# Performance work log

Measured on AMD Instinct MI355X. Metric: run time of the kernel, lower is better.

The kernel has to match this reference:

```python
import jax, jax.numpy as jnp
import numpy as np

HIDDEN = 2048
NUM_HEADS = 16
HEAD_DIM = HIDDEN // NUM_HEADS
INTER = 8192
EPS = 1e-6


def setup_inputs() -> dict:
    key = jax.random.key(0)
    ks = jax.random.split(key, 10)
    s = 0.02
    return {
        "x": jax.random.normal(ks[0], (2, 2048, HIDDEN), dtype=jnp.float32),
        "w_ln1": jnp.ones((HIDDEN,), dtype=jnp.float32),
        "wq": jax.random.normal(ks[1], (HIDDEN, HIDDEN), dtype=jnp.float32) * s,
        "wk": jax.random.normal(ks[2], (HIDDEN, HIDDEN), dtype=jnp.float32) * s,
        "wv": jax.random.normal(ks[3], (HIDDEN, HIDDEN), dtype=jnp.float32) * s,
        "wo": jax.random.normal(ks[4], (HIDDEN, HIDDEN), dtype=jnp.float32) * s,
        "w_ln2": jnp.ones((HIDDEN,), dtype=jnp.float32),
        "wg": jax.random.normal(ks[5], (INTER, HIDDEN), dtype=jnp.float32) * s,
        "wu": jax.random.normal(ks[6], (INTER, HIDDEN), dtype=jnp.float32) * s,
        "wd": jax.random.normal(ks[7], (HIDDEN, INTER), dtype=jnp.float32) * s,
    }


def rmsnorm(x, w):
    rms = jnp.sqrt(jnp.mean(x * x, axis=-1, keepdims=True) + EPS)
    return x / rms * w


def attention(x, wq, wk, wv, wo):
    B, T, C = x.shape
    # weights are [out, in] (torch Linear convention) -> x @ W.T
    q = (x @ wq.T).reshape(B, T, NUM_HEADS, HEAD_DIM)
    k = (x @ wk.T).reshape(B, T, NUM_HEADS, HEAD_DIM)
    v = (x @ wv.T).reshape(B, T, NUM_HEADS, HEAD_DIM)
    scores = jnp.einsum("bqhd,bkhd->bhqk", q, k) / jnp.sqrt(jnp.float32(HEAD_DIM))
    attn = jax.nn.softmax(scores, axis=-1)
    out = jnp.einsum("bhqk,bkhd->bqhd", attn, v).reshape(B, T, C)
    return out @ wo.T


def mlp(x, wg, wu, wd):
    return (jax.nn.silu(x @ wg.T) * (x @ wu.T)) @ wd.T


def reference(x, w_ln1, wq, wk, wv, wo, w_ln2, wg, wu, wd):
    x = x + attention(rmsnorm(x, w_ln1), wq, wk, wv, wo)
    x = x + mlp(rmsnorm(x, w_ln2), wg, wu, wd)
    return x
```

## Files before the change

kernel.cpp:

```cpp
#include <hip/hip_runtime.h>
#include <stdint.h>

typedef unsigned short u16;
typedef unsigned int   u32;
typedef short s16x8 __attribute__((ext_vector_type(8)));
typedef u16   u16x8 __attribute__((ext_vector_type(8)));
typedef u32   u32x4 __attribute__((ext_vector_type(4)));
typedef float f32x4 __attribute__((ext_vector_type(4)));

__device__ __forceinline__ u16 f2bf(float f) {
    u32 u = __float_as_uint(f);
    u32 r = u + 0x7fffu + ((u >> 16) & 1u);
    return (u16)(r >> 16);
}
__device__ __forceinline__ float bf2f(u16 h) {
    return __uint_as_float(((u32)h) << 16);
}

__device__ __forceinline__ u32 cvtpk(float a, float b) {
    u32 r;
    asm("v_cvt_pk_bf16_f32 %0, %1, %2" : "=v"(r) : "v"(a), "v"(b));
    return r;
}
__device__ __forceinline__ void swap32(u32& a, u32& b) {
#if __has_builtin(__builtin_amdgcn_permlane32_swap)
    auto r = __builtin_amdgcn_permlane32_swap(a, b, false, false);
    a = r[0]; b = r[1];
#else
    asm volatile("v_permlane32_swap_b32 %0, %1" : "+v"(a), "+v"(b));
#endif
}
__device__ __forceinline__ void swap16(u32& a, u32& b) {
#if __has_builtin(__builtin_amdgcn_permlane16_swap)
    auto r = __builtin_amdgcn_permlane16_swap(a, b, false, false);
    a = r[0]; b = r[1];
#else
    asm volatile("v_permlane16_swap_b32 %0, %1" : "+v"(a), "+v"(b));
#endif
}

#define GLD16(gp, lp) __builtin_amdgcn_global_load_lds(                          \
    (const __attribute__((address_space(1))) void*)(uintptr_t)(gp),             \
    (__attribute__((address_space(3))) void*)(u32)(uintptr_t)(lp), 16, 0, 0)

#define FENCE asm volatile("" ::: "memory")

template<int N> __device__ __forceinline__ void waitv() {
    if constexpr (N == 0)      asm volatile("s_waitcnt vmcnt(0)" ::: "memory");
    else if constexpr (N == 3) asm volatile("s_waitcnt vmcnt(3)" ::: "memory");
    else                       asm volatile("s_waitcnt vmcnt(4)" ::: "memory");
}

__global__ __launch_bounds__(256)
void cast_w(const float* __restrict__ in, u16* __restrict__ out, int n)
{
    const int i = (blockIdx.x * 256 + threadIdx.x) * 8;
    if (i >= n) return;
    f32x4 a = *(const f32x4*)(in + i);
    f32x4 b = *(const f32x4*)(in + i + 4);
    u16x8 o;
    o[0] = f2bf(a[0]); o[1] = f2bf(a[1]); o[2] = f2bf(a[2]); o[3] = f2bf(a[3]);
    o[4] = f2bf(b[0]); o[5] = f2bf(b[1]); o[6] = f2bf(b[2]); o[7] = f2bf(b[3]);
    *(u16x8*)(out + i) = o;
}

__global__ __launch_bounds__(256)
void rmsnorm_k(const float* __restrict__ x, const float* __restrict__ wln,
               u16* __restrict__ out, int C)
{
    const int row = blockIdx.x;
    const int tid = threadIdx.x;
    const float* xr = x + (size_t)row * C;
    f32x4 a = *(const f32x4*)(xr + tid * 8);
    f32x4 b = *(const f32x4*)(xr + tid * 8 + 4);
    float s = a[0]*a[0] + a[1]*a[1] + a[2]*a[2] + a[3]*a[3]
            + b[0]*b[0] + b[1]*b[1] + b[2]*b[2] + b[3]*b[3];
    #pragma unroll
    for (int off = 1; off < 64; off <<= 1) s += __shfl_xor(s, off);
    __shared__ float red[4];
    if ((tid & 63) == 0) red[tid >> 6] = s;
    __syncthreads();
    float tot = red[0] + red[1] + red[2] + red[3];
    float inv = rsqrtf(tot / (float)C + 1e-6f);
    f32x4 wa = *(const f32x4*)(wln + tid * 8);
    f32x4 wb = *(const f32x4*)(wln + tid * 8 + 4);
    u16x8 o;
    o[0] = f2bf(a[0]*inv*wa[0]); o[1] = f2bf(a[1]*inv*wa[1]);
    o[2] = f2bf(a[2]*inv*wa[2]); o[3] = f2bf(a[3]*inv*wa[3]);
    o[4] = f2bf(b[0]*inv*wb[0]); o[5] = f2bf(b[1]*inv*wb[1]);
    o[6] = f2bf(b[2]*inv*wb[2]); o[7] = f2bf(b[3]*inv*wb[3]);
    *(u16x8*)(out + (size_t)row * C + tid * 8) = o;
}

template<int MODE, int MR>
__global__ __launch_bounds__(512, 1)
void gemm8(const u16* __restrict__ A, const u16* __restrict__ W,
           const float* __restrict__ resid, const u16* __restrict__ aux,
           void* __restrict__ Cout, int M, int N, int K, float scale)
{
    constexpr int BM  = MR * 32;
    constexpr int MR2 = MR / 2;
    constexpr int SRA = MR * 8;
    constexpr int AL  = BM / 128;
    constexpr int WS  = 2 + AL;
    __shared__ __align__(16) u16 lds[2][(BM + 256) * 64];

    const int tid  = threadIdx.x;
    const int lane = tid & 63;
    const int w    = tid >> 6;
    const int wm   = w >> 2;
    const int wn   = w & 3;

    const int gx  = N >> 8;
    const int nwg = gridDim.x;
    const int sid = ((int)blockIdx.x & 7) * (nwg >> 3) + ((int)blockIdx.x >> 3);
    const int brow = (sid / gx) * BM;
    const int bcol = (sid % gx) * 256;

    const int KT = K >> 6;
    const int NI = KT >> 1;

    f32x4 acc[MR][4] = {};

    auto stageA = [&](int buf, int g, int kt) {
        #pragma unroll
        for (int j = 0; j < AL; ++j) {
            const int p   = j * 64 + (tid >> 3);
            const int row = ((p & ~(SRA - 1)) << 1) | (g * SRA) | (p & (SRA - 1));
            const int ch  = (tid & 7) ^ (row & 7);
            const u16* src = A + (size_t)(brow + row) * K + kt * 64 + ch * 8;
            const int p0  = j * 64 + (w << 3);
            const int r0  = ((p0 & ~(SRA - 1)) << 1) | (g * SRA) | (p0 & (SRA - 1));
            GLD16(src, &lds[buf][0] + r0 * 64);
        }
    };
    auto stageB = [&](int buf, int g, int kt) {
        #pragma unroll
        for (int j = 0; j < 2; ++j) {
            const int p   = j * 64 + (tid >> 3);
            const int row = ((p & ~31) << 1) | (g * 32) | (p & 31);
            const int ch  = (tid & 7) ^ (row & 7);
            const u16* src = W + (size_t)(bcol + row) * K + kt * 64 + ch * 8;
            const int p0  = j * 64 + (w << 3);
            const int r0  = ((p0 & ~31) << 1) | (g * 32) | (p0 & 31);
            GLD16(src, &lds[buf][BM * 64] + r0 * 64);
        }
    };

#define LDA(AF, MH, Ab)                                                          \
    _Pragma("unroll") for (int f = 0; f < MR2; ++f)                              \
    _Pragma("unroll") for (int ks = 0; ks < 2; ++ks) {                           \
        const int row = wm * (BM / 2) + (MH) * (BM / 4) + f * 16 + (lane & 15);  \
        const int ch  = (ks * 4 + (lane >> 4)) ^ (row & 7);                      \
        AF[f][ks] = *(const s16x8*)((Ab) + row * 64 + ch * 8);                   \
    }
#define LDB(BQ, NH, Bb)                                                          \
    _Pragma("unroll") for (int g = 0; g < 2; ++g)                                \
    _Pragma("unroll") for (int ks = 0; ks < 2; ++ks) {                           \
        const int row = wn * 64 + (NH) * 32 + g * 16 + (lane & 15);              \
        const int ch  = (ks * 4 + (lane >> 4)) ^ (row & 7);                      \
        BQ[g][ks] = *(const s16x8*)((Bb) + row * 64 + ch * 8);                   \
    }
#define MFQ(AF, BQ, MH, NH)                                                      \
    __builtin_amdgcn_s_setprio(1);                                               \
    _Pragma("unroll") for (int f = 0; f < MR2; ++f)                              \
    _Pragma("unroll") for (int g = 0; g < 2; ++g)                                \
    _Pragma("unroll") for (int ks = 0; ks < 2; ++ks)                             \
        acc[(MH) * MR2 + f][(NH) * 2 + g] =                                      \
            __builtin_amdgcn_mfma_f32_16x16x32_bf16(                             \
                AF[f][ks], BQ[g][ks], acc[(MH) * MR2 + f][(NH) * 2 + g], 0, 0, 0); \
    __builtin_amdgcn_s_setprio(0);
#define BAR1 FENCE; __builtin_amdgcn_s_barrier(); FENCE
#define ENDP asm volatile("s_waitcnt lgkmcnt(0)" ::: "memory");                  \
             FENCE; __builtin_amdgcn_s_barrier(); FENCE

#define KTILE(BUF, S1, S2, S3, S4, W4)                                           \
    {                                                                            \
        const u16* Ab = &lds[BUF][0];                                            \
        const u16* Bb = &lds[BUF][BM * 64];                                      \
        s16x8 afq[MR2][2], bq0[2][2], bq1[2][2];                                 \
        LDA(afq, 0, Ab) LDB(bq0, 0, Bb)                                          \
        S1; BAR1; MFQ(afq, bq0, 0, 0) ENDP;                                      \
        LDB(bq1, 1, Bb)                                                          \
        S2; BAR1; MFQ(afq, bq1, 0, 1) ENDP;                                      \
        LDA(afq, 1, Ab)                                                          \
        S3; BAR1; MFQ(afq, bq1, 1, 1) ENDP;                                      \
        S4; W4; BAR1; MFQ(afq, bq0, 1, 0) ENDP;                                  \
    }

    stageB(0, 0, 0); stageA(0, 1, 0); stageA(0, 0, 0); stageB(0, 1, 0);
    stageB(1, 0, 1); stageA(1, 1, 1);
    waitv<WS>();
    FENCE; __builtin_amdgcn_s_barrier(); FENCE;

    for (int it = 0; it < NI; ++it) {
        const int t1  = 2 * it + 1;
        const int t0n = 2 * it + 2;
        const int t1n = 2 * it + 3;
        const bool s0 = t0n < KT, s1 = t1n < KT;
        const bool last = (it == NI - 1);

        KTILE(0,
              { stageB(1, 1, t1); },
              { stageA(1, 0, t1); },
              { if (s0) stageB(0, 0, t0n); },
              { if (s0) stageA(0, 1, t0n); },
              { if (last) waitv<0>(); else waitv<WS>(); })
        KTILE(1,
              { if (s0) stageA(0, 0, t0n); },
              { if (s0) stageB(0, 1, t0n); },
              { if (s1) stageB(1, 0, t1n); },
              { if (s1) stageA(1, 1, t1n); },
              { if (!last) waitv<WS>(); })
    }
#undef KTILE
#undef LDA
#undef LDB
#undef MFQ
#undef BAR1
#undef ENDP

    const int er = (lane >> 4) * 4;
    const int ec = lane & 15;
    #pragma unroll
    for (int i = 0; i < MR; ++i) {
        #pragma unroll
        for (int j = 0; j < 4; ++j) {
            #pragma unroll
            for (int r = 0; r < 4; ++r) {
                const int row = brow + wm * (BM / 2) + i * 16 + er + r;
                const int col = bcol + wn * 64 + j * 16 + ec;
                const size_t idx = (size_t)row * N + col;
                const float va = acc[i][j][r];
                if (MODE == 0)      ((u16*)Cout)[idx] = f2bf(va);
                else if (MODE == 1) ((u16*)Cout)[idx] = f2bf(va * scale);
                else if (MODE == 2) ((float*)Cout)[idx] = resid[idx] + va;
                else {
                    const float g  = bf2f(aux[idx]);
                    const float sg = g / (1.0f + exp2f(-g * 1.4426950408889634f));
                    ((u16*)Cout)[idx] = f2bf(sg * va);
                }
            }
        }
    }
}

__global__ __launch_bounds__(256, 2)
void flash_attn(const u16* __restrict__ q, const u16* __restrict__ k,
                const u16* __restrict__ vT, u16* __restrict__ o)
{
    __shared__ __align__(16) u16 Kt[2][64 * 128];
    __shared__ __align__(16) u16 Vt[2][128 * 64];
    const int tid  = threadIdx.x;
    const int lane = tid & 63;
    const int w    = tid >> 6;
    const int qtile = blockIdx.x;
    const int bh    = blockIdx.y;
    const int b = bh >> 4, h = bh & 15;
    const size_t head  = ((size_t)b * 2048) * 2048 + (size_t)h * 128;
    const size_t vbase = ((size_t)h * 128) * 4096 + (size_t)b * 2048;

    s16x8 qf[2][4];
    #pragma unroll
    for (int qi = 0; qi < 2; ++qi) {
        const int tq = qtile * 128 + w * 32 + qi * 16 + (lane & 15);
        const u16* qp = q + head + (size_t)tq * 2048 + (lane >> 4) * 8;
        #pragma unroll
        for (int dk = 0; dk < 4; ++dk) qf[qi][dk] = *(const s16x8*)(qp + dk * 32);
    }

    f32x4 oa[2][8] = {};
    float m_r[2] = {-1e30f, -1e30f};
    float l_r[2] = {0.f, 0.f};

    const int krow = tid >> 2;
    const int kc0  = (tid & 3) * 32;
    const int vd   = tid >> 1;
    const int vk0  = (tid & 1) * 32;
    const u16* kg = k + head + (size_t)krow * 2048 + kc0;
    const u16* vg = vT + vbase + (size_t)vd * 4096 + vk0;
    u32 kwo[4], vwo[4];
    #pragma unroll
    for (int c = 0; c < 4; ++c) {
        kwo[c] = (u32)((krow * 256 + (kc0 + c * 8) * 2) ^ ((krow & 7) << 4));
        vwo[c] = (u32)((vd * 128 + (vk0 + c * 8) * 2)   ^ ((vd & 7) << 4));
    }

    s16x8 kr[4], vr[4];
    #pragma unroll
    for (int c = 0; c < 4; ++c) {
        kr[c] = *(const s16x8*)(kg + c * 8);
        vr[c] = *(const s16x8*)(vg + c * 8);
    }

    for (int kb = 0; kb < 32; ++kb) {
        const int cur = kb & 1;
        char* KtB = (char*)&Kt[cur][0];
        char* VtB = (char*)&Vt[cur][0];
        #pragma unroll
        for (int c = 0; c < 4; ++c) {
            *(s16x8*)(KtB + kwo[c]) = kr[c];
            *(s16x8*)(VtB + vwo[c]) = vr[c];
        }
        if (kb + 1 < 32) {
            const int k0n = (kb + 1) * 64;
            #pragma unroll
            for (int c = 0; c < 4; ++c) {
                kr[c] = *(const s16x8*)(kg + (size_t)k0n * 2048 + c * 8);
                vr[c] = *(const s16x8*)(vg + k0n + c * 8);
            }
        }
        asm volatile("s_waitcnt lgkmcnt(0)" ::: "memory");
        __builtin_amdgcn_s_barrier();
        FENCE;

        f32x4 st[2][4] = {};
        __builtin_amdgcn_s_setprio(1);
        #pragma unroll
        for (int kt = 0; kt < 4; ++kt) {
            const int row = kt * 16 + (lane & 15);
            s16x8 kf[4];
            #pragma unroll
            for (int dk = 0; dk < 4; ++dk) {
                const int dcol = dk * 32 + (lane >> 4) * 8;
                kf[dk] = *(const s16x8*)(KtB + ((row * 256 + dcol * 2) ^ ((row & 7) << 4)));
            }
            #pragma unroll
            for (int qi = 0; qi < 2; ++qi)
                #pragma unroll
                for (int dk = 0; dk < 4; ++dk)
                    st[qi][kt] = __builtin_amdgcn_mfma_f32_16x16x32_bf16(kf[dk], qf[qi][dk], st[qi][kt], 0, 0, 0);
        }
        __builtin_amdgcn_s_setprio(0);

        float mx[2];
        #pragma unroll
        for (int qi = 0; qi < 2; ++qi) {
            float m0 = fmaxf(fmaxf(st[qi][0][0], st[qi][0][1]), fmaxf(st[qi][0][2], st[qi][0][3]));
            float m1 = fmaxf(fmaxf(st[qi][1][0], st[qi][1][1]), fmaxf(st[qi][1][2], st[qi][1][3]));
            float m2 = fmaxf(fmaxf(st[qi][2][0], st[qi][2][1]), fmaxf(st[qi][2][2], st[qi][2][3]));
            float m3 = fmaxf(fmaxf(st[qi][3][0], st[qi][3][1]), fmaxf(st[qi][3][2], st[qi][3][3]));
            float m0123 = fmaxf(fmaxf(m0, m1), fmaxf(m2, m3));
            m0123 = fmaxf(m0123, __shfl_xor(m0123, 16));
            m0123 = fmaxf(m0123, __shfl_xor(m0123, 32));
            mx[qi] = m0123;
        }
        const bool grow = (mx[0] > m_r[0] + 8.f) || (mx[1] > m_r[1] + 8.f);
        if (__any(grow)) {
            #pragma unroll
            for (int qi = 0; qi < 2; ++qi) {
                const float mn = fmaxf(m_r[qi], mx[qi]);
                const float sc = exp2f(m_r[qi] - mn);
                m_r[qi] = mn;
                l_r[qi] *= sc;
                const float s0 = __shfl(sc, (lane >> 4) * 4 + 0);
                const float s1 = __shfl(sc, (lane >> 4) * 4 + 1);
                const float s2 = __shfl(sc, (lane >> 4) * 4 + 2);
                const float s3 = __shfl(sc, (lane >> 4) * 4 + 3);
                #pragma unroll
                for (int ni = 0; ni < 8; ++ni) {
                    oa[qi][ni][0] *= s0; oa[qi][ni][1] *= s1;
                    oa[qi][ni][2] *= s2; oa[qi][ni][3] *= s3;
                }
            }
        }

        s16x8 pa[2][2];
        #pragma unroll
        for (int qi = 0; qi < 2; ++qi) {
            float sum = 0.f;
            #pragma unroll
            for (int kt = 0; kt < 4; ++kt)
                #pragma unroll
                for (int r = 0; r < 4; ++r) {
                    const float p = exp2f(st[qi][kt][r] - m_r[qi]);
                    st[qi][kt][r] = p;
                    sum += p;
                }
            sum += __shfl_xor(sum, 16);
            sum += __shfl_xor(sum, 32);
            l_r[qi] += sum;

            u32 q01[4], q23[4];
            #pragma unroll
            for (int kt = 0; kt < 4; ++kt) {
                q01[kt] = cvtpk(st[qi][kt][0], st[qi][kt][1]);
                q23[kt] = cvtpk(st[qi][kt][2], st[qi][kt][3]);
            }
            #pragma unroll
            for (int ks = 0; ks < 2; ++ks) {
                u32 X = q01[2 * ks], Y = q01[2 * ks + 1];
                swap32(X, Y); swap16(X, Y);
                u32 U = q23[2 * ks], V = q23[2 * ks + 1];
                swap32(U, V); swap16(U, V);
                u32x4 t; t[0] = X; t[1] = U; t[2] = Y; t[3] = V;
                pa[qi][ks] = __builtin_bit_cast(s16x8, t);
            }
        }

        __builtin_amdgcn_s_setprio(1);
        #pragma unroll
        for (int ks = 0; ks < 2; ++ks) {
            const int keyb = ks * 32 + (lane >> 4) * 8;
            #pragma unroll
            for (int ni = 0; ni < 8; ++ni) {
                const int dd = ni * 16 + (lane & 15);
                s16x8 vf = *(const s16x8*)(VtB + ((dd * 128 + keyb * 2) ^ ((dd & 7) << 4)));
                #pragma unroll
                for (int qi = 0; qi < 2; ++qi)
                    oa[qi][ni] = __builtin_amdgcn_mfma_f32_16x16x32_bf16(pa[qi][ks], vf, oa[qi][ni], 0, 0, 0);
            }
        }
        __builtin_amdgcn_s_setprio(0);
    }
    #pragma unroll
    for (int qi = 0; qi < 2; ++qi) {
        #pragma unroll
        for (int r = 0; r < 4; ++r) {
            const float inv = 1.0f / __shfl(l_r[qi], (lane >> 4) * 4 + r);
            const int tout = qtile * 128 + w * 32 + qi * 16 + (lane >> 4) * 4 + r;
            u16* op = o + head + (size_t)tout * 2048 + (lane & 15);
            #pragma unroll
            for (int ni = 0; ni < 8; ++ni)
                op[ni * 16] = f2bf(oa[qi][ni][r] * inv);
        }
    }
}

extern "C" void kernel_launch(void* const* d_in, const int* in_sizes, int n_in,
                              void* d_out, int out_size, void* d_ws, size_t ws_size,
                              hipStream_t stream)
{
    (void)in_sizes; (void)n_in; (void)out_size; (void)ws_size;
    const float* x    = (const float*)d_in[0];
    const float* wln1 = (const float*)d_in[1];
    const float* wq   = (const float*)d_in[2];
    const float* wk   = (const float*)d_in[3];
    const float* wv   = (const float*)d_in[4];
    const float* wo   = (const float*)d_in[5];
    const float* wln2 = (const float*)d_in[6];
    const float* wg   = (const float*)d_in[7];
    const float* wu   = (const float*)d_in[8];
    const float* wd   = (const float*)d_in[9];
    float* out = (float*)d_out;

    const size_t MB = 1024ull * 1024ull;
    char* ws = (char*)d_ws;
    u16*   arena = (u16*)(ws + 0);
    float* hbuf  = (float*)(ws + 32 * MB);
    u16*   xn    = (u16*)(ws + 64 * MB);
    u16*   qb    = (u16*)(ws + 80 * MB);
    u16*   kbuf  = (u16*)(ws + 96 * MB);
    u16*   vT    = (u16*)(ws + 112 * MB);
    u16*   abuf  = (u16*)(ws + 128 * MB);
    u16*   gbuf  = (u16*)(ws + 80 * MB);

    const int M = 4096, C = 2048, I = 8192;
    const float qscale = 0.1275164899f;
    dim3 blk(256);
    dim3 blk8(512);

    rmsnorm_k<<<M, blk, 0, stream>>>(x, wln1, xn, C);

    cast_w<<<(C * C) / 2048, blk, 0, stream>>>(wq, arena, C * C);
    gemm8<1, 4><<<dim3((C / 256) * (M / 128)), blk8, 0, stream>>>(xn, arena, nullptr, nullptr, qb, M, C, C, qscale);
    cast_w<<<(C * C) / 2048, blk, 0, stream>>>(wk, arena, C * C);
    gemm8<0, 4><<<dim3((C / 256) * (M / 128)), blk8, 0, stream>>>(xn, arena, nullptr, nullptr, kbuf, M, C, C, 1.f);
    cast_w<<<(C * C) / 2048, blk, 0, stream>>>(wv, arena, C * C);
    gemm8<0, 4><<<dim3((M / 256) * (C / 128)), blk8, 0, stream>>>(arena, xn, nullptr, nullptr, vT, C, M, C, 1.f);

    flash_attn<<<dim3(2048 / 128, 32), blk, 0, stream>>>(qb, kbuf, vT, abuf);

    cast_w<<<(C * C) / 2048, blk, 0, stream>>>(wo, arena, C * C);
    gemm8<2, 4><<<dim3((C / 256) * (M / 128)), blk8, 0, stream>>>(abuf, arena, x, nullptr, hbuf, M, C, C, 1.f);

    rmsnorm_k<<<M, blk, 0, stream>>>(hbuf, wln2, xn, C);

    cast_w<<<(I * C) / 2048, blk, 0, stream>>>(wg, arena, I * C);
    gemm8<0, 8><<<dim3((I / 256) * (M / 256)), blk8, 0, stream>>>(xn, arena, nullptr, nullptr, gbuf, M, I, C, 1.f);
    cast_w<<<(I * C) / 2048, blk, 0, stream>>>(wu, arena, I * C);
    gemm8<3, 8><<<dim3((I / 256) * (M / 256)), blk8, 0, stream>>>(xn, arena, nullptr, gbuf, gbuf, M, I, C, 1.f);
    cast_w<<<(C * I) / 2048, blk, 0, stream>>>(wd, arena, C * I);
    gemm8<2, 4><<<dim3((C / 256) * (M / 128)), blk8, 0, stream>>>(gbuf, arena, hbuf, nullptr, out, M, C, I, 1.f);
}
```

Measured before the change: 719.3 us.

## Restructure GEMM K-loop into single-barrier phases with prefetched LDS fragments

Reworks the main GEMM K-loop schedule so each quarter-tile phase uses one barrier followed by an lgkmcnt wait instead of two barriers. Fragments for the next phase are loaded from LDS ahead of time, and the global-to-LDS staging order and vmcnt wait depths are reshuffled (vmcnt(2) instead of 3/4). The aim is to cut barrier overhead and overlap LDS reads with MFMA work. The risk lies in the correctness of the buffer reuse ordering, since the staging order for the last tile and half-buffer overlaps is subtle.

Result: no change. 717.9 us (-0.2%).

```diff
diff --git a/kernel.cpp b/kernel.cpp
--- a/kernel.cpp
+++ b/kernel.cpp
@@ -47,6 +47,7 @@
 
 template<int N> __device__ __forceinline__ void waitv() {
     if constexpr (N == 0)      asm volatile("s_waitcnt vmcnt(0)" ::: "memory");
+    else if constexpr (N == 2) asm volatile("s_waitcnt vmcnt(2)" ::: "memory");
     else if constexpr (N == 3) asm volatile("s_waitcnt vmcnt(3)" ::: "memory");
     else                       asm volatile("s_waitcnt vmcnt(4)" ::: "memory");
 }
@@ -102,7 +103,6 @@
     constexpr int MR2 = MR / 2;
     constexpr int SRA = MR * 8;
     constexpr int AL  = BM / 128;
-    constexpr int WS  = 2 + AL;
     __shared__ __align__(16) u16 lds[2][(BM + 256) * 64];
 
     const int tid  = threadIdx.x;
@@ -147,19 +147,19 @@
         }
     };
 
-#define LDA(AF, MH, Ab)                                                          \
+#define LDAF(AF, MH, BUF)                                                        \
     _Pragma("unroll") for (int f = 0; f < MR2; ++f)                              \
     _Pragma("unroll") for (int ks = 0; ks < 2; ++ks) {                           \
         const int row = wm * (BM / 2) + (MH) * (BM / 4) + f * 16 + (lane & 15);  \
         const int ch  = (ks * 4 + (lane >> 4)) ^ (row & 7);                      \
-        AF[f][ks] = *(const s16x8*)((Ab) + row * 64 + ch * 8);                   \
-    }
-#define LDB(BQ, NH, Bb)                                                          \
+        AF[f][ks] = *(const s16x8*)(&lds[BUF][0] + row * 64 + ch * 8);           \
+    }
+#define LDBF(BQ, NH, BUF)                                                        \
     _Pragma("unroll") for (int g = 0; g < 2; ++g)                                \
     _Pragma("unroll") for (int ks = 0; ks < 2; ++ks) {                           \
         const int row = wn * 64 + (NH) * 32 + g * 16 + (lane & 15);              \
         const int ch  = (ks * 4 + (lane >> 4)) ^ (row & 7);                      \
-        BQ[g][ks] = *(const s16x8*)((Bb) + row * 64 + ch * 8);                   \
+        BQ[g][ks] = *(const s16x8*)(&lds[BUF][BM * 64] + row * 64 + ch * 8);     \
     }
 #define MFQ(AF, BQ, MH, NH)                                                      \
     __builtin_amdgcn_s_setprio(1);                                               \
@@ -170,55 +170,54 @@
             __builtin_amdgcn_mfma_f32_16x16x32_bf16(                             \
                 AF[f][ks], BQ[g][ks], acc[(MH) * MR2 + f][(NH) * 2 + g], 0, 0, 0); \
     __builtin_amdgcn_s_setprio(0);
-#define BAR1 FENCE; __builtin_amdgcn_s_barrier(); FENCE
-#define ENDP asm volatile("s_waitcnt lgkmcnt(0)" ::: "memory");                  \
-             FENCE; __builtin_amdgcn_s_barrier(); FENCE
-
-#define KTILE(BUF, S1, S2, S3, S4, W4)                                           \
-    {                                                                            \
-        const u16* Ab = &lds[BUF][0];                                            \
-        const u16* Bb = &lds[BUF][BM * 64];                                      \
-        s16x8 afq[MR2][2], bq0[2][2], bq1[2][2];                                 \
-        LDA(afq, 0, Ab) LDB(bq0, 0, Bb)                                          \
-        S1; BAR1; MFQ(afq, bq0, 0, 0) ENDP;                                      \
-        LDB(bq1, 1, Bb)                                                          \
-        S2; BAR1; MFQ(afq, bq1, 0, 1) ENDP;                                      \
-        LDA(afq, 1, Ab)                                                          \
-        S3; BAR1; MFQ(afq, bq1, 1, 1) ENDP;                                      \
-        S4; W4; BAR1; MFQ(afq, bq0, 1, 0) ENDP;                                  \
-    }
-
-    stageB(0, 0, 0); stageA(0, 1, 0); stageA(0, 0, 0); stageB(0, 1, 0);
-    stageB(1, 0, 1); stageA(1, 1, 1);
-    waitv<WS>();
+#define PH_ENTRY FENCE; __builtin_amdgcn_s_barrier();                            \
+    asm volatile("s_waitcnt lgkmcnt(0)" ::: "memory"); FENCE
+
+    s16x8 af[MR2][2], bqA[2][2], bqB[2][2];
+
+    stageB(0, 0, 0); stageA(0, 0, 0); stageB(0, 1, 0); stageA(0, 1, 0);
+    stageB(1, 0, 1); stageA(1, 0, 1); stageB(1, 1, 1);
+    waitv<0>();
     FENCE; __builtin_amdgcn_s_barrier(); FENCE;
+    LDAF(af, 0, 0) LDBF(bqA, 0, 0)
 
     for (int it = 0; it < NI; ++it) {
         const int t1  = 2 * it + 1;
         const int t0n = 2 * it + 2;
         const int t1n = 2 * it + 3;
-        const bool s0 = t0n < KT, s1 = t1n < KT;
         const bool last = (it == NI - 1);
 
-        KTILE(0,
-              { stageB(1, 1, t1); },
-              { stageA(1, 0, t1); },
-              { if (s0) stageB(0, 0, t0n); },
-              { if (s0) stageA(0, 1, t0n); },
-              { if (last) waitv<0>(); else waitv<WS>(); })
-        KTILE(1,
-              { if (s0) stageA(0, 0, t0n); },
-              { if (s0) stageB(0, 1, t0n); },
-              { if (s1) stageB(1, 0, t1n); },
-              { if (s1) stageA(1, 1, t1n); },
-              { if (!last) waitv<WS>(); })
-    }
-#undef KTILE
-#undef LDA
-#undef LDB
+        PH_ENTRY; MFQ(af, bqA, 0, 0)
+        LDBF(bqB, 1, 0)
+        stageA(1, 1, t1);
+        PH_ENTRY; MFQ(af, bqB, 0, 1)
+        LDAF(af, 1, 0)
+        if (!last) stageB(0, 0, t0n);
+        PH_ENTRY; MFQ(af, bqB, 1, 1)
+        if (!last) stageA(0, 0, t0n);
+        PH_ENTRY; MFQ(af, bqA, 1, 0)
+        if (!last) stageB(0, 1, t0n);
+        if (last) { waitv<0>(); } else { waitv<2>(); }
+        LDAF(af, 0, 1) LDBF(bqA, 0, 1)
+        PH_ENTRY; MFQ(af, bqA, 0, 0)
+        LDBF(bqB, 1, 1)
+        if (!last) stageA(0, 1, t0n);
+        PH_ENTRY; MFQ(af, bqB, 0, 1)
+        LDAF(af, 1, 1)
+        if (!last) stageB(1, 0, t1n);
+        PH_ENTRY; MFQ(af, bqB, 1, 1)
+        if (!last) stageA(1, 0, t1n);
+        PH_ENTRY; MFQ(af, bqA, 1, 0)
+        if (!last) {
+            stageB(1, 1, t1n);
+            waitv<2>();
+            LDAF(af, 0, 0) LDBF(bqA, 0, 0)
+        }
+    }
+#undef LDAF
+#undef LDBF
 #undef MFQ
-#undef BAR1
-#undef ENDP
+#undef PH_ENTRY
 
     const int er = (lane >> 4) * 4;
     const int ec = lane & 15;
```
